# Kernel optimization log

Hardware: AMD Instinct MI355X
Metric: run time of the kernel (lower is better)

## Reference

```python
import jax, jax.numpy as jnp
import numpy as np

EPS = 1e-12


def pairwise_sqdist(x, y):
    # x: (B, N, 3), y: (B, M, 3) -> (B, N, M) squared euclidean distances
    xx = jnp.sum(x * x, axis=-1)              # (B, N)
    yy = jnp.sum(y * y, axis=-1)              # (B, M)
    xy = jnp.einsum('bnd,bmd->bnm', x, y)     # (B, N, M)
    d = xx[:, :, None] + yy[None_ if False else yy[:, None, :].shape and 0 or ...] if False else xx[:, :, None] + yy[:, None, :] - 2.0 * xy
    return jnp.maximum(d, 0.0)


def chamfer_l1(x, y):
    # pytorch3d/PoinTr-style ChamferDistanceL1:
    # mean over points of sqrt(min squared dist), averaged over both directions
    d = pairwise_sqdist(x, y)                 # (B, N, M)
    d1 = jnp.min(d, axis=2)                   # (B, N) x -> nearest y
    d2 = jnp.min(d, axis=1)                   # (B, M) y -> nearest x
    d1 = jnp.sqrt(jnp.maximum(d1, EPS))
    d2 = jnp.sqrt(jnp.maximum(d2, EPS))
    return 0.5 * (jnp.mean(d1) + jnp.mean(d2))


def knn1_gather(x, y):
    # For each point in x (B,N,3), find nearest neighbor in y (B,M,3) (K=1)
    # and gather it -> (B, N, 3). Matches knn_points + knn_gather + squeeze.
    d = pairwise_sqdist(x, y)                 # (B, N, M)
    idx = jnp.argmin(d, axis=2)               # (B, N) int
    return jnp.take_along_axis(y, idx[:, :, None], axis=1)  # (B, N, 3)


def volume_with_wedge(p):
    # wedge-product volume over consecutive point triples:
    # V = sum_i (p_i x p_{i+1}) . p_{i+2} / 6  -> (B,)
    c = jnp.cross(p[:, :-2, :], p[:, 1:-1, :])  # (B, N-2, 3)
    return jnp.sum(jnp.einsum('bnd,bnd->bn', c, p[:, 2:, :]), axis=-1) / 6.0


def setup_inputs() -> dict:
    key = jax.random.key(0)
    k1, k2, k3 = jax.random.split(key, 3)
    B, Nc, Nf, M = 2, 512, 8192, 8192
    return {
        'source_coarse': jax.random.normal(k1, (B, Nc, 3), dtype=jnp.float32),
        'source_fine': jax.random.normal(k2, (B, Nf, 3), dtype=jnp.float32),
        'target_points': jax.random.normal(k3, (B, M, 3), dtype=jnp.float32),
    }


def reference(source_coarse, source_fine, target_points):
    lambda_rot = lambda_ref = lambda_align = lambda_geo = 1.0
    B = source_fine.shape[0]
    axis = jnp.broadcast_to(jnp.array([0.0, 0.0, 1.0], dtype=source_fine.dtype), (B, 3))
    plane_normal = jnp.broadcast_to(jnp.array([0.0, 1.0, 0.0], dtype=source_fine.dtype), (B, 3))

    # KNN (K=1) gather of nearest target point for each fine source point
    new_target = knn1_gather(source_fine, target_points)  # (B, Nf, 3)

    # alignment (Chamfer L1) losses
    loss_align_coarse = chamfer_l1(source_coarse, target_points)
    loss_align_fine = chamfer_l1(source_fine, target_points)

    # rotational symmetry loss
    in_proj = jnp.einsum('bij,bj->bi', source_fine, axis)      # (B, Nf)
    re_proj = jnp.einsum('bij,bj->bi', new_target, axis)
    loss_rot = jnp.mean((jnp.linalg.norm(in_proj, axis=-1) - jnp.linalg.norm(re_proj, axis=-1)) ** 2)

    # reflectional symmetry loss
    pn = plane_normal / jnp.linalg.norm(plane_normal, axis=-1, keepdims=True)
    in_dist = jnp.einsum('bij,bj->bi', source_fine, pn)
    re_dist = jnp.einsum('bij,bj->bi', new_target, pn)
    loss_ref = jnp.mean((in_dist - re_dist) ** 2)

    # geometric consistency (wedge-product volume) loss
    loss_geo = jnp.mean((volume_with_wedge(source_fine) - volume_with_wedge(new_target)) ** 2)

    total = (lambda_rot * loss_rot + lambda_ref * loss_ref
             + lambda_align * loss_align_coarse + lambda_align * loss_align_fine
             + lambda_geo * loss_geo)
    return total
```

## Files before the change

kernel.cpp:

```cpp
#include <hip/hip_runtime.h>
#include <stdint.h>
#include <float.h>

using u64 = unsigned long long;
typedef float v2f __attribute__((ext_vector_type(2)));

constexpr int B_ = 2;
constexpr int NC = 512;
constexpr int NF = 8192;
constexpr int MT = 8192;

constexpr int TPB = 256;
constexpr int RPB = 512;
constexpr int CF  = 16;
constexpr int CFC = 8;
constexpr int TAIL_BLOCKS = 196;

#define DEVINL __device__ __forceinline__

__global__ __launch_bounds__(TPB) void prep(
    const float* __restrict__ coarse, const float* __restrict__ fine,
    const float* __restrict__ tgt,
    float4* __restrict__ fine4, float4* __restrict__ tgt4,
    float4* __restrict__ coarse4, unsigned* __restrict__ counter)
{
#pragma clang fp contract(off)
    int g = blockIdx.x * TPB + threadIdx.x;
    if (g == 0) *counter = 0;
    if (g < B_ * NF) {
        const float* p = fine + (size_t)g * 3;
        float x = p[0], y = p[1], z = p[2];
        fine4[g] = make_float4(x, y, z, (x*x + y*y) + z*z);
        p = tgt + (size_t)g * 3;
        x = p[0]; y = p[1]; z = p[2];
        tgt4[g] = make_float4(x, y, z, (x*x + y*y) + z*z);
        if (g < B_ * NC) {
            p = coarse + (size_t)g * 3;
            x = p[0]; y = p[1]; z = p[2];
            coarse4[g] = make_float4(x, y, z, (x*x + y*y) + z*z);
        }
    }
}

template<bool ARGMIN>
DEVINL void pairmin_body(const float* __restrict__ P, const float4* __restrict__ Qf,
                         int nP, int nQb, int b, int row_base, int j0, int jlen,
                         int chunk, int nRowsTot,
                         u64* __restrict__ outPack, unsigned* __restrict__ outVal)
{
#pragma clang fp contract(off)
    const int tid  = threadIdx.x;
    const int row0 = row_base + tid;
    const int row1 = row_base + tid + TPB;
    const float* p0 = P + ((size_t)b * nP + row0) * 3;
    const float* p1 = P + ((size_t)b * nP + row1) * 3;
    float a0 = p0[0], a1 = p0[1], a2 = p0[2];
    float e0 = p1[0], e1 = p1[1], e2 = p1[2];
    v2f tx0 = {2.0f * a0, 2.0f * e0};
    v2f tx1 = {2.0f * a1, 2.0f * e1};
    v2f tx2 = {2.0f * a2, 2.0f * e2};
    v2f txx = {(a0*a0 + a1*a1) + a2*a2, (e0*e0 + e1*e1) + e2*e2};
    v2f dbest = {FLT_MAX, FLT_MAX};
    const v2f vzero = {0.0f, 0.0f};
    int jb0 = 0, jb1 = 0;

    const float4* Q = Qf + (size_t)b * nQb;
    float4 c0 = Q[j0], c1 = Q[j0+1], c2 = Q[j0+2], c3 = Q[j0+3];

    for (int j = j0; j < j0 + jlen; j += 4) {
        float4 n0 = Q[j+4], n1 = Q[j+5], n2 = Q[j+6], n3 = Q[j+7];
        float4 qg[4] = {c0, c1, c2, c3};
        #pragma unroll
        for (int u = 0; u < 4; ++u) {
            float4 q = qg[u];
            v2f s  = (tx0 * q.x + tx1 * q.y) + tx2 * q.z;
            v2f tt = txx + q.w;
            v2f d  = tt - s;
            v2f dc = __builtin_elementwise_max(d, vzero);
            if (ARGMIN) {
                int jj = j + u;
                bool g0 = dc.x < dbest.x;
                dbest.x = g0 ? dc.x : dbest.x;  jb0 = g0 ? jj : jb0;
                bool g1 = dc.y < dbest.y;
                dbest.y = g1 ? dc.y : dbest.y;  jb1 = g1 ? jj : jb1;
            } else {
                dbest = __builtin_elementwise_min(dbest, dc);
            }
        }
        c0 = n0; c1 = n1; c2 = n2; c3 = n3;
    }

    const size_t o0 = (size_t)chunk * nRowsTot + (size_t)b * nP;
    if (ARGMIN) {
        outPack[o0 + row0] = ((u64)__float_as_uint(dbest.x) << 32) | (unsigned)jb0;
        outPack[o0 + row1] = ((u64)__float_as_uint(dbest.y) << 32) | (unsigned)jb1;
    } else {
        outVal[o0 + row0] = __float_as_uint(dbest.x);
        outVal[o0 + row1] = __float_as_uint(dbest.y);
    }
}

__global__ __launch_bounds__(TPB, 8) void pairmin_all(
    const float* __restrict__ coarse, const float* __restrict__ fine,
    const float* __restrict__ tgt,
    const float4* __restrict__ fine4, const float4* __restrict__ tgt4,
    const float4* __restrict__ coarse4,
    u64* __restrict__ pfr, unsigned* __restrict__ pfc,
    unsigned* __restrict__ pcr, unsigned* __restrict__ pcc)
{
    const int bx = blockIdx.x;
    if (bx < 256) {
        int chunk = bx & 7, yb = (bx >> 3) & 15, b = bx >> 7;
        pairmin_body<false>(tgt, fine4, MT, NF, b, yb * RPB, chunk * 1024, 1024,
                            chunk, B_ * MT, nullptr, pfc);
    } else if (bx < 768) {
        int i = bx - 256;
        int chunk = i & 15, yb = (i >> 4) & 15, b = i >> 8;
        pairmin_body<true>(fine, tgt4, NF, MT, b, yb * RPB, chunk * 512, 512,
                           chunk, B_ * NF, pfr, nullptr);
    } else if (bx < 800) {
        int i = bx - 768;
        int chunk = i & 15, b = i >> 4;
        pairmin_body<false>(coarse, tgt4, NC, MT, b, 0, chunk * 512, 512,
                            chunk, B_ * NC, nullptr, pcr);
    } else {
        int i = bx - 800;
        int yb = i & 15, b = i >> 4;
        pairmin_body<false>(tgt, coarse4, MT, NC, b, yb * RPB, 0, 512,
                            0, B_ * MT, nullptr, pcc);
    }
}

__global__ __launch_bounds__(TPB) void tail_all(
    const float* __restrict__ fine, const float* __restrict__ tgt,
    const u64* __restrict__ pfr, const unsigned* __restrict__ pfc,
    const unsigned* __restrict__ pcr, const unsigned* __restrict__ pcc,
    double* __restrict__ bs, unsigned* __restrict__ counter,
    float* __restrict__ out)
{
    __shared__ float sp[TPB + 2][3], yp[TPB + 2][3];
    __shared__ double redw[4][9];
    __shared__ double lred[4][13];
    __shared__ int lastflag;
    const int bx = blockIdx.x, tid = threadIdx.x;
    const int wave = tid >> 6, lane = tid & 63;

    double v_s = 0, v_d2f = 0, v_d1c = 0, v_d2c = 0, v_yd2 = 0, v_zs = 0, v_zt = 0;
    double vs = 0, vt = 0;
    int role_b = 0;

    if (bx < 64) {
        const int base = bx * TPB;
        const int g = base + tid;
        const int b = base >> 13;  role_b = b;
        u64 best = pfr[g];
        #pragma unroll
        for (int c = 1; c < CF; ++c) {
            u64 p = pfr[(size_t)c * (B_ * NF) + g];
            best = p < best ? p : best;
        }
        float d1 = __uint_as_float((unsigned)(best >> 32));
        int idx  = (int)(best & 0xffffffffULL);
        float s = sqrtf(fmaxf(d1, 1e-12f));
        const float* y  = tgt  + ((size_t)b * MT + idx) * 3;
        const float* sr = fine + (size_t)g * 3;
        float y0 = y[0],  y1 = y[1],  y2 = y[2];
        float s0 = sr[0], s1 = sr[1], s2 = sr[2];
        yp[tid][0] = y0; yp[tid][1] = y1; yp[tid][2] = y2;
        sp[tid][0] = s0; sp[tid][1] = s1; sp[tid][2] = s2;
        const int base_b = base & (NF - 1);
        if (tid < 2 && base_b + TPB + tid < NF) {
            int g2 = base + TPB + tid;
            u64 b2 = pfr[g2];
            #pragma unroll
            for (int c = 1; c < CF; ++c) {
                u64 p = pfr[(size_t)c * (B_ * NF) + g2];
                b2 = p < b2 ? p : b2;
            }
            int i2 = (int)(b2 & 0xffffffffULL);
            const float* yh = tgt  + ((size_t)b * MT + i2) * 3;
            const float* sh = fine + (size_t)g2 * 3;
            #pragma unroll
            for (int k = 0; k < 3; ++k) { yp[TPB + tid][k] = yh[k]; sp[TPB + tid][k] = sh[k]; }
        }
        __syncthreads();
        v_s = s;
        float yd = s1 - y1;
        v_yd2 = (double)(yd * yd);
        v_zs  = (double)(s2 * s2);
        v_zt  = (double)(y2 * y2);
        int rb = base_b + tid;
        if (rb <= NF - 3) {
            {
                const float* a = sp[tid]; const float* c = sp[tid+1]; const float* e = sp[tid+2];
                float c0 = a[1]*c[2] - a[2]*c[1];
                float c1 = a[2]*c[0] - a[0]*c[2];
                float c2 = a[0]*c[1] - a[1]*c[0];
                vs = (double)(c0*e[0] + c1*e[1] + c2*e[2]);
            }
            {
                const float* a = yp[tid]; const float* c = yp[tid+1]; const float* e = yp[tid+2];
                float c0 = a[1]*c[2] - a[2]*c[1];
                float c1 = a[2]*c[0] - a[0]*c[2];
                float c2 = a[0]*c[1] - a[1]*c[0];
                vt = (double)(c0*e[0] + c1*e[1] + c2*e[2]);
            }
        }
    } else if (bx < 128) {
        const int g = (bx - 64) * TPB + tid;
        unsigned best = pfc[g];
        #pragma unroll
        for (int c = 1; c < CFC; ++c) best = min(best, pfc[(size_t)c * (B_ * MT) + g]);
        v_d2f = (double)sqrtf(fmaxf(__uint_as_float(best), 1e-12f));
    } else if (bx < 132) {
        const int g = (bx - 128) * TPB + tid;
        unsigned best = pcr[g];
        #pragma unroll
        for (int c = 1; c < 16; ++c) best = min(best, pcr[(size_t)c * (B_ * NC) + g]);
        v_d1c = (double)sqrtf(fmaxf(__uint_as_float(best), 1e-12f));
    } else {
        const int g = (bx - 132) * TPB + tid;
        v_d2c = (double)sqrtf(fmaxf(__uint_as_float(pcc[g]), 1e-12f));
    }

    double r9[9] = {v_s, v_d2f, v_d1c, v_d2c, v_yd2, v_zs, v_zt, vs, vt};
    for (int o = 32; o; o >>= 1) {
        #pragma unroll
        for (int k = 0; k < 9; ++k) r9[k] += __shfl_down(r9[k], o);
    }
    if (lane == 0) {
        #pragma unroll
        for (int k = 0; k < 9; ++k) redw[wave][k] = r9[k];
    }
    __syncthreads();
    if (tid == 0) {
        double t9[9];
        #pragma unroll
        for (int k = 0; k < 9; ++k)
            t9[k] = redw[0][k] + redw[1][k] + redw[2][k] + redw[3][k];
        double* o = bs + (size_t)bx * 16;
        #pragma unroll
        for (int k = 0; k < 16; ++k) o[k] = 0.0;
        o[0] = t9[0]; o[1] = t9[1]; o[2] = t9[2]; o[3] = t9[3]; o[4] = t9[4];
        o[5 + role_b]  = t9[5];
        o[7 + role_b]  = t9[6];
        o[9 + role_b]  = t9[7];
        o[11 + role_b] = t9[8];
        __threadfence();
        unsigned old = atomicAdd(counter, 1u);
        lastflag = (old == TAIL_BLOCKS - 1);
    }
    __syncthreads();
    if (!lastflag) return;

    __threadfence();
    double c13[13];
    if (tid < TAIL_BLOCKS) {
        const double* p = bs + (size_t)tid * 16;
        #pragma unroll
        for (int k = 0; k < 13; ++k) c13[k] = p[k];
    } else {
        #pragma unroll
        for (int k = 0; k < 13; ++k) c13[k] = 0.0;
    }
    for (int o = 32; o; o >>= 1) {
        #pragma unroll
        for (int k = 0; k < 13; ++k) c13[k] += __shfl_down(c13[k], o);
    }
    if (lane == 0) {
        #pragma unroll
        for (int k = 0; k < 13; ++k) lred[wave][k] = c13[k];
    }
    __syncthreads();
    if (tid == 0) {
        double S[13];
        #pragma unroll
        for (int k = 0; k < 13; ++k)
            S[k] = lred[0][k] + lred[1][k] + lred[2][k] + lred[3][k];
        double m_d1f = S[0] / (double)(B_ * NF);
        double m_d2f = S[1] / (double)(B_ * MT);
        double m_d1c = S[2] / (double)(B_ * NC);
        double m_d2c = S[3] / (double)(B_ * MT);
        double loss_align_fine   = 0.5 * (m_d1f + m_d2f);
        double loss_align_coarse = 0.5 * (m_d1c + m_d2c);
        double loss_ref = S[4] / (double)(B_ * NF);
        double loss_rot = 0.0, loss_geo = 0.0;
        for (int b = 0; b < B_; ++b) {
            double dn = sqrt(S[5 + b]) - sqrt(S[7 + b]);
            loss_rot += dn * dn;
            double dv = (S[9 + b] - S[11 + b]) / 6.0;
            loss_geo += dv * dv;
        }
        loss_rot /= (double)B_;
        loss_geo /= (double)B_;
        out[0] = (float)(loss_rot + loss_ref + loss_align_coarse + loss_align_fine + loss_geo);
    }
}

extern "C" void kernel_launch(void* const* d_in, const int* in_sizes, int n_in,
                              void* d_out, int out_size, void* d_ws, size_t ws_size,
                              hipStream_t stream)
{
    const float* src_coarse = (const float*)d_in[0];
    const float* src_fine   = (const float*)d_in[1];
    const float* tgt        = (const float*)d_in[2];
    float* out = (float*)d_out;
    char*  ws  = (char*)d_ws;

    u64*      pfr     = (u64*)(ws);
    unsigned* pfc     = (unsigned*)(ws + 2097152);
    unsigned* pcr     = (unsigned*)(ws + 2621440);
    unsigned* pcc     = (unsigned*)(ws + 2686976);
    float4*   fine4   = (float4*)(ws + 2752512);
    float4*   tgt4    = (float4*)(ws + 3014656);
    float4*   coarse4 = (float4*)(ws + 3276800);
    double*   bs      = (double*)(ws + 3293184);
    unsigned* counter = (unsigned*)(ws + 3318272);

    prep<<<dim3(64), TPB, 0, stream>>>(src_coarse, src_fine, tgt,
                                       fine4, tgt4, coarse4, counter);
    pairmin_all<<<dim3(832), TPB, 0, stream>>>(
        src_coarse, src_fine, tgt, fine4, tgt4, coarse4, pfr, pfc, pcr, pcc);
    tail_all<<<dim3(TAIL_BLOCKS), TPB, 0, stream>>>(
        src_fine, tgt, pfr, pfc, pcr, pcc, bs, counter, out);
}
```

Before: 135.0 us.

## Pair query points in SoA layout and use packed ops with scalar operands

The preprocessed point arrays are laid out as interleaved pairs (x0,x1,y0,y1,z0,z1,w0,w1), so each thread handles one row against two columns at a time with packed-f32 inline asm that takes the column data as SGPR operands. Each thread now owns one row instead of two, the grid grows to more blocks with smaller column chunks, and the fine-to-target chamfer now splits columns into 16 chunks instead of 8. The non-argmin path folds the clamp-to-zero and the running minimum into a single fmed3. The intent is to load column data once per wave through scalar loads and cut vector register and instruction pressure. It relies on the compiler placing the column values in SGPRs as the inline-asm constraints require, and the wider chunking adds partial-result traffic for the tail reduction.

```diff
diff --git a/kernel.cpp b/kernel.cpp
--- a/kernel.cpp
+++ b/kernel.cpp
@@ -11,123 +11,132 @@
 constexpr int MT = 8192;
 
 constexpr int TPB = 256;
-constexpr int RPB = 512;
 constexpr int CF  = 16;
-constexpr int CFC = 8;
 constexpr int TAIL_BLOCKS = 196;
 
 #define DEVINL __device__ __forceinline__
+
+DEVINL v2f pk_mul_vs(v2f a, v2f b){ v2f d; asm("v_pk_mul_f32 %0, %1, %2" : "=v"(d) : "v"(a), "s"(b)); return d; }
+DEVINL v2f pk_add_vv(v2f a, v2f b){ v2f d; asm("v_pk_add_f32 %0, %1, %2" : "=v"(d) : "v"(a), "v"(b)); return d; }
+DEVINL v2f pk_add_vs(v2f a, v2f b){ v2f d; asm("v_pk_add_f32 %0, %1, %2" : "=v"(d) : "v"(a), "s"(b)); return d; }
 
 __global__ __launch_bounds__(TPB) void prep(
     const float* __restrict__ coarse, const float* __restrict__ fine,
     const float* __restrict__ tgt,
-    float4* __restrict__ fine4, float4* __restrict__ tgt4,
-    float4* __restrict__ coarse4, unsigned* __restrict__ counter)
+    float* __restrict__ finep, float* __restrict__ tgtp,
+    float* __restrict__ coarsep, unsigned* __restrict__ counter)
 {
 #pragma clang fp contract(off)
     int g = blockIdx.x * TPB + threadIdx.x;
     if (g == 0) *counter = 0;
-    if (g < B_ * NF) {
-        const float* p = fine + (size_t)g * 3;
-        float x = p[0], y = p[1], z = p[2];
-        fine4[g] = make_float4(x, y, z, (x*x + y*y) + z*z);
-        p = tgt + (size_t)g * 3;
-        x = p[0]; y = p[1]; z = p[2];
-        tgt4[g] = make_float4(x, y, z, (x*x + y*y) + z*z);
-        if (g < B_ * NC) {
-            p = coarse + (size_t)g * 3;
-            x = p[0]; y = p[1]; z = p[2];
-            coarse4[g] = make_float4(x, y, z, (x*x + y*y) + z*z);
+    if (g < B_ * NF / 2) {
+        {
+            const float* p = fine + (size_t)g * 6;
+            float x0=p[0],y0=p[1],z0=p[2],x1=p[3],y1=p[4],z1=p[5];
+            float* o = finep + (size_t)g * 8;
+            o[0]=x0; o[1]=x1; o[2]=y0; o[3]=y1; o[4]=z0; o[5]=z1;
+            o[6]=(x0*x0+y0*y0)+z0*z0;  o[7]=(x1*x1+y1*y1)+z1*z1;
+        }
+        {
+            const float* p = tgt + (size_t)g * 6;
+            float x0=p[0],y0=p[1],z0=p[2],x1=p[3],y1=p[4],z1=p[5];
+            float* o = tgtp + (size_t)g * 8;
+            o[0]=x0; o[1]=x1; o[2]=y0; o[3]=y1; o[4]=z0; o[5]=z1;
+            o[6]=(x0*x0+y0*y0)+z0*z0;  o[7]=(x1*x1+y1*y1)+z1*z1;
+        }
+        if (g < B_ * NC / 2) {
+            const float* p = coarse + (size_t)g * 6;
+            float x0=p[0],y0=p[1],z0=p[2],x1=p[3],y1=p[4],z1=p[5];
+            float* o = coarsep + (size_t)g * 8;
+            o[0]=x0; o[1]=x1; o[2]=y0; o[3]=y1; o[4]=z0; o[5]=z1;
+            o[6]=(x0*x0+y0*y0)+z0*z0;  o[7]=(x1*x1+y1*y1)+z1*z1;
         }
     }
 }
 
 template<bool ARGMIN>
-DEVINL void pairmin_body(const float* __restrict__ P, const float4* __restrict__ Qf,
-                         int nP, int nQb, int b, int row_base, int j0, int jlen,
-                         int chunk, int nRowsTot,
+DEVINL void pairmin_body(const float* __restrict__ P, const v2f* __restrict__ Qp,
+                         int nP, int nQpairsB, int b, int row_base,
+                         int jp0, int jplen, int chunk, int nRowsTot,
                          u64* __restrict__ outPack, unsigned* __restrict__ outVal)
 {
 #pragma clang fp contract(off)
-    const int tid  = threadIdx.x;
-    const int row0 = row_base + tid;
-    const int row1 = row_base + tid + TPB;
-    const float* p0 = P + ((size_t)b * nP + row0) * 3;
-    const float* p1 = P + ((size_t)b * nP + row1) * 3;
-    float a0 = p0[0], a1 = p0[1], a2 = p0[2];
-    float e0 = p1[0], e1 = p1[1], e2 = p1[2];
-    v2f tx0 = {2.0f * a0, 2.0f * e0};
-    v2f tx1 = {2.0f * a1, 2.0f * e1};
-    v2f tx2 = {2.0f * a2, 2.0f * e2};
-    v2f txx = {(a0*a0 + a1*a1) + a2*a2, (e0*e0 + e1*e1) + e2*e2};
-    v2f dbest = {FLT_MAX, FLT_MAX};
-    const v2f vzero = {0.0f, 0.0f};
+    const int tid = threadIdx.x;
+    const int row = row_base + tid;
+    const float* p = P + ((size_t)b * nP + row) * 3;
+    float a0 = p[0], a1 = p[1], a2 = p[2];
+    v2f vax = {-2.0f * a0, -2.0f * a0};
+    v2f vay = {-2.0f * a1, -2.0f * a1};
+    v2f vaz = {-2.0f * a2, -2.0f * a2};
+    float xx = (a0*a0 + a1*a1) + a2*a2;
+    v2f vxx = {xx, xx};
+    float db0 = FLT_MAX, db1 = FLT_MAX;
     int jb0 = 0, jb1 = 0;
 
-    const float4* Q = Qf + (size_t)b * nQb;
-    float4 c0 = Q[j0], c1 = Q[j0+1], c2 = Q[j0+2], c3 = Q[j0+3];
-
-    for (int j = j0; j < j0 + jlen; j += 4) {
-        float4 n0 = Q[j+4], n1 = Q[j+5], n2 = Q[j+6], n3 = Q[j+7];
-        float4 qg[4] = {c0, c1, c2, c3};
-        #pragma unroll
-        for (int u = 0; u < 4; ++u) {
-            float4 q = qg[u];
-            v2f s  = (tx0 * q.x + tx1 * q.y) + tx2 * q.z;
-            v2f tt = txx + q.w;
-            v2f d  = tt - s;
-            v2f dc = __builtin_elementwise_max(d, vzero);
-            if (ARGMIN) {
-                int jj = j + u;
-                bool g0 = dc.x < dbest.x;
-                dbest.x = g0 ? dc.x : dbest.x;  jb0 = g0 ? jj : jb0;
-                bool g1 = dc.y < dbest.y;
-                dbest.y = g1 ? dc.y : dbest.y;  jb1 = g1 ? jj : jb1;
-            } else {
-                dbest = __builtin_elementwise_min(dbest, dc);
-            }
-        }
-        c0 = n0; c1 = n1; c2 = n2; c3 = n3;
-    }
-
-    const size_t o0 = (size_t)chunk * nRowsTot + (size_t)b * nP;
+    const v2f* Q = Qp + ((size_t)b * nQpairsB + jp0) * 4;
+    v2f qx = Q[0], qy = Q[1], qz = Q[2], qw = Q[3];
+    int j = jp0 * 2;
+    for (int k = 0; k < jplen; ++k) {
+        const v2f* Qn = Q + (size_t)(k + 1) * 4;
+        v2f nx = Qn[0], ny = Qn[1], nz = Qn[2], nw = Qn[3];
+        v2f m0  = pk_mul_vs(vax, qx);
+        v2f m1  = pk_mul_vs(vay, qy);
+        v2f m2  = pk_mul_vs(vaz, qz);
+        v2f s01 = pk_add_vv(m0, m1);
+        v2f sxy = pk_add_vv(s01, m2);
+        v2f tt  = pk_add_vs(vxx, qw);
+        v2f d   = pk_add_vv(tt, sxy);
+        if (ARGMIN) {
+            float c0 = fmaxf(d.x, 0.0f);
+            float c1 = fmaxf(d.y, 0.0f);
+            bool t0 = c0 < db0;  db0 = t0 ? c0 : db0;  jb0 = t0 ? j     : jb0;
+            bool t1 = c1 < db1;  db1 = t1 ? c1 : db1;  jb1 = t1 ? (j+1) : jb1;
+        } else {
+            db0 = __builtin_amdgcn_fmed3f(d.x, 0.0f, db0);
+            db1 = __builtin_amdgcn_fmed3f(d.y, 0.0f, db1);
+        }
+        qx = nx; qy = ny; qz = nz; qw = nw;
+        j += 2;
+    }
+    const size_t o = (size_t)chunk * nRowsTot + (size_t)b * nP + row;
     if (ARGMIN) {
-        outPack[o0 + row0] = ((u64)__float_as_uint(dbest.x) << 32) | (unsigned)jb0;
-        outPack[o0 + row1] = ((u64)__float_as_uint(dbest.y) << 32) | (unsigned)jb1;
+        bool odd = (db1 < db0) || (db1 == db0 && jb1 < jb0);
+        float db = odd ? db1 : db0;
+        int   jb = odd ? jb1 : jb0;
+        outPack[o] = ((u64)__float_as_uint(db) << 32) | (unsigned)jb;
     } else {
-        outVal[o0 + row0] = __float_as_uint(dbest.x);
-        outVal[o0 + row1] = __float_as_uint(dbest.y);
+        outVal[o] = __float_as_uint(fminf(db0, db1));
     }
 }
 
 __global__ __launch_bounds__(TPB, 8) void pairmin_all(
     const float* __restrict__ coarse, const float* __restrict__ fine,
     const float* __restrict__ tgt,
-    const float4* __restrict__ fine4, const float4* __restrict__ tgt4,
-    const float4* __restrict__ coarse4,
+    const v2f* __restrict__ finep, const v2f* __restrict__ tgtp,
+    const v2f* __restrict__ coarsep,
     u64* __restrict__ pfr, unsigned* __restrict__ pfc,
     unsigned* __restrict__ pcr, unsigned* __restrict__ pcc)
 {
     const int bx = blockIdx.x;
-    if (bx < 256) {
-        int chunk = bx & 7, yb = (bx >> 3) & 15, b = bx >> 7;
-        pairmin_body<false>(tgt, fine4, MT, NF, b, yb * RPB, chunk * 1024, 1024,
-                            chunk, B_ * MT, nullptr, pfc);
-    } else if (bx < 768) {
-        int i = bx - 256;
-        int chunk = i & 15, yb = (i >> 4) & 15, b = i >> 8;
-        pairmin_body<true>(fine, tgt4, NF, MT, b, yb * RPB, chunk * 512, 512,
-                           chunk, B_ * NF, pfr, nullptr);
-    } else if (bx < 800) {
-        int i = bx - 768;
-        int chunk = i & 15, b = i >> 4;
-        pairmin_body<false>(coarse, tgt4, NC, MT, b, 0, chunk * 512, 512,
-                            chunk, B_ * NC, nullptr, pcr);
+    if (bx < 1024) {
+        int chunk = bx & 15, yb = (bx >> 4) & 31, b = bx >> 9;
+        pairmin_body<false>(tgt, finep, MT, NF/2, b, yb*TPB, chunk*256, 256,
+                            chunk, B_*MT, nullptr, pfc);
+    } else if (bx < 2048) {
+        int i = bx - 1024;
+        int chunk = i & 15, yb = (i >> 4) & 31, b = i >> 9;
+        pairmin_body<true>(fine, tgtp, NF, MT/2, b, yb*TPB, chunk*256, 256,
+                           chunk, B_*NF, pfr, nullptr);
+    } else if (bx < 2112) {
+        int i = bx - 2048;
+        int chunk = i & 15, yb = (i >> 4) & 1, b = i >> 5;
+        pairmin_body<false>(coarse, tgtp, NC, MT/2, b, yb*TPB, chunk*256, 256,
+                            chunk, B_*NC, nullptr, pcr);
     } else {
-        int i = bx - 800;
-        int yb = i & 15, b = i >> 4;
-        pairmin_body<false>(tgt, coarse4, MT, NC, b, yb * RPB, 0, 512,
-                            0, B_ * MT, nullptr, pcc);
+        int i = bx - 2112;
+        int yb = i & 31, b = i >> 5;
+        pairmin_body<false>(tgt, coarsep, MT, NC/2, b, yb*TPB, 0, 256,
+                            0, B_*MT, nullptr, pcc);
     }
 }
 
@@ -210,7 +219,7 @@
         const int g = (bx - 64) * TPB + tid;
         unsigned best = pfc[g];
         #pragma unroll
-        for (int c = 1; c < CFC; ++c) best = min(best, pfc[(size_t)c * (B_ * MT) + g]);
+        for (int c = 1; c < CF; ++c) best = min(best, pfc[(size_t)c * (B_ * MT) + g]);
         v_d2f = (double)sqrtf(fmaxf(__uint_as_float(best), 1e-12f));
     } else if (bx < 132) {
         const int g = (bx - 128) * TPB + tid;
@@ -309,18 +318,20 @@
 
     u64*      pfr     = (u64*)(ws);
     unsigned* pfc     = (unsigned*)(ws + 2097152);
-    unsigned* pcr     = (unsigned*)(ws + 2621440);
-    unsigned* pcc     = (unsigned*)(ws + 2686976);
-    float4*   fine4   = (float4*)(ws + 2752512);
-    float4*   tgt4    = (float4*)(ws + 3014656);
-    float4*   coarse4 = (float4*)(ws + 3276800);
-    double*   bs      = (double*)(ws + 3293184);
-    unsigned* counter = (unsigned*)(ws + 3318272);
-
-    prep<<<dim3(64), TPB, 0, stream>>>(src_coarse, src_fine, tgt,
-                                       fine4, tgt4, coarse4, counter);
-    pairmin_all<<<dim3(832), TPB, 0, stream>>>(
-        src_coarse, src_fine, tgt, fine4, tgt4, coarse4, pfr, pfc, pcr, pcc);
+    unsigned* pcr     = (unsigned*)(ws + 3145728);
+    unsigned* pcc     = (unsigned*)(ws + 3211264);
+    float*    finep   = (float*)(ws + 3276800);
+    float*    tgtp    = (float*)(ws + 3538944);
+    float*    coarsep = (float*)(ws + 3801088);
+    double*   bs      = (double*)(ws + 3817472);
+    unsigned* counter = (unsigned*)(ws + 3842560);
+
+    prep<<<dim3(32), TPB, 0, stream>>>(src_coarse, src_fine, tgt,
+                                       finep, tgtp, coarsep, counter);
+    pairmin_all<<<dim3(2176), TPB, 0, stream>>>(
+        src_coarse, src_fine, tgt,
+        (const v2f*)finep, (const v2f*)tgtp, (const v2f*)coarsep,
+        pfr, pfc, pcr, pcc);
     tail_all<<<dim3(TAIL_BLOCKS), TPB, 0, stream>>>(
         src_fine, tgt, pfr, pfc, pcr, pcc, bs, counter, out);
 }
```

After: 132.8 us. Within noise of the previous version (-1.6%).
